# Performance work log

Hardware: AMD Instinct MI355X
Metric: run time of the kernel (lower is better)

Reference implementation:

```python
import jax, jax.numpy as jnp
import numpy as np

DIM = 768
HEADS = 12
HEAD_DIM = DIM // HEADS
HIDDEN = int(DIM * 2.0)
EPS = 1e-5


def layer_norm(x, g, b):
    mu = jnp.mean(x, axis=-1, keepdims=True)
    var = jnp.var(x, axis=-1, keepdims=True)
    return (x - mu) * jax.lax.rsqrt(var + EPS) * g + b


def setup_inputs() -> dict:
    key = jax.random.key(0)
    ks = jax.random.split(key, 10)
    B, N = 8, 1024
    s = 0.02
    return {
        "x": jax.random.normal(ks[0], (B, N, DIM), jnp.float32),
        "rpe_bias": jax.random.normal(ks[1], (HEADS, N, N), jnp.float32),
        # weights stored as (in, out); equals torch Linear weight transposed
        "qkv_w": jax.random.normal(ks[2], (DIM, 3 * DIM), jnp.float32) * s,
        "proj_w": jax.random.normal(ks[3], (DIM, DIM), jnp.float32) * s,
        "proj_b": jnp.zeros((DIM,), jnp.float32),
        "ln1_g": jnp.ones((DIM,), jnp.float32),
        "ln1_b": jnp.zeros((DIM,), jnp.float32),
        "ln2_g": jnp.ones((DIM,), jnp.float32),
        "ln2_b": jnp.zeros((DIM,), jnp.float32),
        "fc1_w": jax.random.normal(ks[4], (DIM, HIDDEN), jnp.float32) * s,
        "fc1_b": jnp.zeros((HIDDEN,), jnp.float32),
        "fc2_w": jax.random.normal(ks[5], (HIDDEN, DIM), jnp.float32) * s,
        "fc2_b": jnp.zeros((DIM,), jnp.float32),
    }


def reference(x, rpe_bias, qkv_w, proj_w, proj_b, ln1_g, ln1_b, ln2_g, ln2_b,
              fc1_w, fc1_b, fc2_w, fc2_b):
    B, N, C = x.shape
    scale = HEAD_DIM ** -0.5

    # ---- attention branch (pre-norm) ----
    h = layer_norm(x, ln1_g, ln1_b)
    qkv = h @ qkv_w                                   # [B,N,3C]
    qkv = qkv.reshape(B, N, 3, HEADS, HEAD_DIM)
    q = jnp.transpose(qkv[:, :, 0], (0, 2, 1, 3))     # [B,H,N,D]
    k = jnp.transpose(qkv[:, :, 1], (0, 2, 1, 3))
    v = jnp.transpose(qkv[:, :, 2], (0, 2, 1, 3))
    attn = jnp.einsum('bhnd,bhmd->bhnm', q, k) * scale + rpe_bias[None]
    attn = jax.nn.softmax(attn, axis=-1)
    o = jnp.einsum('bhnm,bhmd->bhnd', attn, v)        # [B,H,N,D]
    o = jnp.transpose(o, (0, 2, 1, 3)).reshape(B, N, C)
    x = x + (o @ proj_w + proj_b)

    # ---- MLP branch (pre-norm) ----
    h = layer_norm(x, ln2_g, ln2_b)
    h = jax.nn.gelu(h @ fc1_w + fc1_b, approximate=False)
    x = x + (h @ fc2_w + fc2_b)
    return x
```

## Files before the change

kernel.cpp:

```cpp
#include <hip/hip_runtime.h>

typedef __bf16 bf16;
typedef __bf16 bf16x8 __attribute__((ext_vector_type(8)));
typedef float f32x4 __attribute__((ext_vector_type(4)));

#define DIM 768
#define HEADS 12
#define HD 64
#define HIDDEN 1536
#define BB 8
#define NN 1024
#define ROWS (BB*NN)

__device__ __forceinline__ void gload_lds16(const void* g, void* l) {
  __builtin_amdgcn_global_load_lds(
      (const __attribute__((address_space(1))) void*)g,
      (__attribute__((address_space(3))) void*)l, 16, 0, 0);
}

__global__ __launch_bounds__(256) void rpe_cvt_kernel(
    const float* __restrict__ in, bf16* __restrict__ out)
{
  const size_t total = (size_t)HEADS * NN * NN;
  const size_t stride = (size_t)gridDim.x * 256 * 4;
  for (size_t i = ((size_t)blockIdx.x * 256 + threadIdx.x) * 4; i < total; i += stride) {
    const float4 v = *(const float4*)(in + i);
    ushort4 u;
    u.x = __builtin_bit_cast(unsigned short, (bf16)v.x);
    u.y = __builtin_bit_cast(unsigned short, (bf16)v.y);
    u.z = __builtin_bit_cast(unsigned short, (bf16)v.z);
    u.w = __builtin_bit_cast(unsigned short, (bf16)v.w);
    *(ushort4*)(out + i) = u;
  }
}

__global__ __launch_bounds__(256) void ln_kernel(
    const float* __restrict__ x, const float* __restrict__ gw,
    const float* __restrict__ bw, bf16* __restrict__ out)
{
  const int row = blockIdx.x;
  const int tid = threadIdx.x;
  const float* xr = x + (size_t)row * DIM;
  float v0 = xr[tid], v1 = xr[tid + 256], v2 = xr[tid + 512];
  float s1 = v0 + v1 + v2;
  float s2 = v0*v0 + v1*v1 + v2*v2;
#pragma unroll
  for (int off = 1; off < 64; off <<= 1) {
    s1 += __shfl_xor(s1, off);
    s2 += __shfl_xor(s2, off);
  }
  __shared__ float red[8];
  const int w = tid >> 6, lane = tid & 63;
  if (lane == 0) { red[w] = s1; red[4 + w] = s2; }
  __syncthreads();
  s1 = red[0] + red[1] + red[2] + red[3];
  s2 = red[4] + red[5] + red[6] + red[7];
  const float mu = s1 * (1.f / DIM);
  const float rstd = rsqrtf(s2 * (1.f / DIM) - mu * mu + 1e-5f);
  bf16* orow = out + (size_t)row * DIM;
  orow[tid]       = (bf16)((v0 - mu) * rstd * gw[tid]       + bw[tid]);
  orow[tid + 256] = (bf16)((v1 - mu) * rstd * gw[tid + 256] + bw[tid + 256]);
  orow[tid + 512] = (bf16)((v2 - mu) * rstd * gw[tid + 512] + bw[tid + 512]);
}

__global__ void wtrans_kernel(const float* __restrict__ in, bf16* __restrict__ out,
                              int K, int N)
{
  __shared__ float t[32][33];
  const int tx = threadIdx.x, ty = threadIdx.y;
  const int n0 = blockIdx.x * 32, k0 = blockIdx.y * 32;
#pragma unroll
  for (int i = 0; i < 32; i += 8)
    t[ty + i][tx] = in[(size_t)(k0 + ty + i) * N + n0 + tx];
  __syncthreads();
#pragma unroll
  for (int i = 0; i < 32; i += 8)
    out[(size_t)(n0 + ty + i) * K + k0 + tx] = (bf16)t[tx][ty + i];
}

template<int EPI>
__global__ __launch_bounds__(256, 2) void gemm128(
    const bf16* __restrict__ A, const bf16* __restrict__ Bt,
    int M, int N, int K,
    const float* __restrict__ bias, const float* __restrict__ resid,
    void* __restrict__ o0, void* __restrict__ o1, void* __restrict__ o2)
{
  __shared__ bf16 sA[128 * 64];
  __shared__ bf16 sB[128 * 64];
  const int tid = threadIdx.x;
  const int lane = tid & 63, w = tid >> 6;
  const int wrow = w >> 1, wcol = w & 1;
  const int m0 = blockIdx.y * 128, n0 = blockIdx.x * 128;
  const int l15 = lane & 15, l4 = lane >> 4;

  f32x4 acc[4][4] = {};

  const int crow = lane >> 3;
  const int cbyte = (lane & 7) * 16;
  const int ksteps = K >> 6;
  for (int kt = 0; kt < ksteps; ++kt) {
    const int k0 = kt << 6;
    __syncthreads();
#pragma unroll
    for (int c2 = 0; c2 < 4; ++c2) {
      const int c = (w << 2) + c2;
      const int r = (c << 3) + crow;
      gload_lds16((const char*)(A + (size_t)(m0 + r) * K + k0) + cbyte,
                  (char*)sA + c * 1024);
      gload_lds16((const char*)(Bt + (size_t)(n0 + r) * K + k0) + cbyte,
                  (char*)sB + c * 1024);
    }
    __syncthreads();
#pragma unroll
    for (int kk = 0; kk < 64; kk += 32) {
      bf16x8 af[4], bfv[4];
#pragma unroll
      for (int mf = 0; mf < 4; ++mf)
        af[mf] = *(const bf16x8*)(sA + (wrow * 64 + mf * 16 + l15) * 64 + kk + l4 * 8);
#pragma unroll
      for (int nf = 0; nf < 4; ++nf)
        bfv[nf] = *(const bf16x8*)(sB + (wcol * 64 + nf * 16 + l15) * 64 + kk + l4 * 8);
#pragma unroll
      for (int mf = 0; mf < 4; ++mf)
#pragma unroll
        for (int nf = 0; nf < 4; ++nf)
          acc[mf][nf] = __builtin_amdgcn_mfma_f32_16x16x32_bf16(af[mf], bfv[nf], acc[mf][nf], 0, 0, 0);
    }
  }

#pragma unroll
  for (int mf = 0; mf < 4; ++mf) {
    const int rbase = m0 + wrow * 64 + mf * 16 + l4 * 4;
#pragma unroll
    for (int nf = 0; nf < 4; ++nf) {
      const int colbase = n0 + wcol * 64 + nf * 16;
      const int col = colbase + l15;
      if constexpr (EPI == 0) {
        const int seg = colbase / 768;
        const int hh_ = (colbase - seg * 768) >> 6;
        const int dd = (colbase & 63) + l15;
        const int b_ = rbase >> 10;
        const int ns = rbase & 1023;
        const size_t gh = (size_t)(b_ * HEADS + hh_);
        bf16* Qb = (bf16*)o0; bf16* Kb = (bf16*)o1; bf16* Vtb = (bf16*)o2;
        if (seg == 0) {
#pragma unroll
          for (int rg = 0; rg < 4; ++rg)
            Qb[(gh * NN + ns + rg) * HD + dd] = (bf16)(acc[mf][nf][rg] * 0.125f);
        } else if (seg == 1) {
#pragma unroll
          for (int rg = 0; rg < 4; ++rg)
            Kb[(gh * NN + ns + rg) * HD + dd] = (bf16)acc[mf][nf][rg];
        } else {
          union { ushort4 u4; unsigned short us[4]; } pk;
#pragma unroll
          for (int rg = 0; rg < 4; ++rg)
            pk.us[rg] = __builtin_bit_cast(unsigned short, (bf16)acc[mf][nf][rg]);
          *(ushort4*)(Vtb + (gh * HD + dd) * NN + ns) = pk.u4;
        }
      } else if constexpr (EPI == 1 || EPI == 3) {
        float* outp = (float*)o0;
#pragma unroll
        for (int rg = 0; rg < 4; ++rg) {
          const size_t idx = (size_t)(rbase + rg) * N + col;
          outp[idx] = acc[mf][nf][rg] + bias[col] + resid[idx];
        }
      } else {
        bf16* outp = (bf16*)o0;
#pragma unroll
        for (int rg = 0; rg < 4; ++rg) {
          float v = acc[mf][nf][rg] + bias[col];
          float gl = 0.5f * v * (1.0f + erff(v * 0.70710678118654752f));
          outp[(size_t)(rbase + rg) * N + col] = (bf16)gl;
        }
      }
    }
  }
}

__global__ __launch_bounds__(256, 4) void attn_kernel(
    const bf16* __restrict__ Qb, const bf16* __restrict__ Kb,
    const bf16* __restrict__ Vtb, const bf16* __restrict__ rpeb,
    bf16* __restrict__ o_attn)
{
  __shared__ bf16 sK[2][64 * 64];
  __shared__ bf16 sV[2][64 * 64];
  __shared__ bf16 sP[4 * 16 * 64];
  const int tid = threadIdx.x;
  const int lane = tid & 63, w = tid >> 6;
  const int l15 = lane & 15, l4 = lane >> 4;
  const int bid = blockIdx.x;
  const int g = bid >> 4, qt = bid & 15;
  const int b_ = g / HEADS, h_ = g % HEADS;
  const int qbase = qt * 64 + w * 16;

  bf16x8 qf[2];
  {
    const bf16* qp = Qb + ((size_t)g * NN + qbase + l15) * HD + l4 * 8;
    qf[0] = *(const bf16x8*)qp;
    qf[1] = *(const bf16x8*)(qp + 32);
  }

  f32x4 oacc[4] = {};
  float m_r[4] = {-1e30f, -1e30f, -1e30f, -1e30f};
  float l_r[4] = {};
  const bf16* rpe_h = rpeb + (size_t)h_ * NN * NN;

  const int crow = lane >> 3;
  const int scol = ((lane & 7) * 16) ^ ((crow & 7) << 4);
  const int cc = w * 2;

#define STAGE(buf, kv0s) do {                                                      \
    _Pragma("unroll")                                                              \
    for (int c2 = 0; c2 < 2; ++c2) {                                               \
      const int c = cc + c2;                                                       \
      const int r = c * 8 + crow;                                                  \
      gload_lds16((const char*)(Kb + ((size_t)g * NN + (kv0s)) * HD) + r * 128 + scol, \
                  (char*)sK[buf] + c * 1024);                                      \
      gload_lds16((const char*)(Vtb + ((size_t)g * HD + r) * NN + (kv0s)) + scol,  \
                  (char*)sV[buf] + c * 1024);                                      \
    } } while (0)

  STAGE(0, 0);
  __syncthreads();
  int cur = 0;

  for (int kv0 = 0; kv0 < NN; kv0 += 64) {
    if (kv0 + 64 < NN) STAGE(cur ^ 1, kv0 + 64);

    float rv[4][4];
#pragma unroll
    for (int nf = 0; nf < 4; ++nf)
#pragma unroll
      for (int rg = 0; rg < 4; ++rg)
        rv[nf][rg] = (float)rpe_h[(size_t)(qbase + l4 * 4 + rg) * NN + kv0 + nf * 16 + l15];

    f32x4 s[4] = {};
#pragma unroll
    for (int kh = 0; kh < 2; ++kh) {
#pragma unroll
      for (int nf = 0; nf < 4; ++nf) {
        const int n_ = nf * 16 + l15;
        const bf16x8 kf = *(const bf16x8*)((const char*)sK[cur] + n_ * 128 +
                            (((kh * 32 + l4 * 8) * 2) ^ ((n_ & 7) << 4)));
        s[nf] = __builtin_amdgcn_mfma_f32_16x16x32_bf16(qf[kh], kf, s[nf], 0, 0, 0);
      }
    }
    float rm[4] = {-1e30f, -1e30f, -1e30f, -1e30f};
#pragma unroll
    for (int nf = 0; nf < 4; ++nf)
#pragma unroll
      for (int rg = 0; rg < 4; ++rg) {
        float v = s[nf][rg] + rv[nf][rg];
        s[nf][rg] = v;
        rm[rg] = fmaxf(rm[rg], v);
      }
#pragma unroll
    for (int off = 1; off <= 8; off <<= 1)
#pragma unroll
      for (int rg = 0; rg < 4; ++rg)
        rm[rg] = fmaxf(rm[rg], __shfl_xor(rm[rg], off));
    float al[4];
#pragma unroll
    for (int rg = 0; rg < 4; ++rg) {
      const float mn = fmaxf(m_r[rg], rm[rg]);
      al[rg] = __expf(m_r[rg] - mn);
      m_r[rg] = mn;
    }
    float rs[4] = {};
#pragma unroll
    for (int nf = 0; nf < 4; ++nf)
#pragma unroll
      for (int rg = 0; rg < 4; ++rg) {
        const float p = __expf(s[nf][rg] - m_r[rg]);
        rs[rg] += p;
        const int r = l4 * 4 + rg;
        const int cb = (nf * 16 + l15) * 2;
        *(bf16*)((char*)sP + w * 2048 + r * 128 + (cb ^ ((r & 7) << 4))) = (bf16)p;
      }
#pragma unroll
    for (int off = 1; off <= 8; off <<= 1)
#pragma unroll
      for (int rg = 0; rg < 4; ++rg)
        rs[rg] += __shfl_xor(rs[rg], off);
#pragma unroll
    for (int rg = 0; rg < 4; ++rg)
      l_r[rg] = l_r[rg] * al[rg] + rs[rg];
#pragma unroll
    for (int df = 0; df < 4; ++df)
#pragma unroll
      for (int rg = 0; rg < 4; ++rg)
        oacc[df][rg] *= al[rg];

#pragma unroll
    for (int kh = 0; kh < 2; ++kh) {
      const bf16x8 pf = *(const bf16x8*)((const char*)sP + w * 2048 + l15 * 128 +
                          (((kh * 32 + l4 * 8) * 2) ^ ((l15 & 7) << 4)));
#pragma unroll
      for (int df = 0; df < 4; ++df) {
        const int d_ = df * 16 + l15;
        const bf16x8 vf = *(const bf16x8*)((const char*)sV[cur] + d_ * 128 +
                            (((kh * 32 + l4 * 8) * 2) ^ ((d_ & 7) << 4)));
        oacc[df] = __builtin_amdgcn_mfma_f32_16x16x32_bf16(pf, vf, oacc[df], 0, 0, 0);
      }
    }
    __syncthreads();
    cur ^= 1;
  }
#undef STAGE

#pragma unroll
  for (int rg = 0; rg < 4; ++rg) {
    const float inv = 1.0f / l_r[rg];
    const int qr = qbase + l4 * 4 + rg;
    bf16* orow = o_attn + ((size_t)(b_ * NN) + qr) * DIM + h_ * HD;
#pragma unroll
    for (int df = 0; df < 4; ++df)
      orow[df * 16 + l15] = (bf16)(oacc[df][rg] * inv);
  }
}

extern "C" void kernel_launch(void* const* d_in, const int* in_sizes, int n_in,
                              void* d_out, int out_size, void* d_ws, size_t ws_size,
                              hipStream_t stream)
{
  const float* x      = (const float*)d_in[0];
  const float* rpe    = (const float*)d_in[1];
  const float* qkv_w  = (const float*)d_in[2];
  const float* proj_w = (const float*)d_in[3];
  const float* proj_b = (const float*)d_in[4];
  const float* ln1_g  = (const float*)d_in[5];
  const float* ln1_b  = (const float*)d_in[6];
  const float* ln2_g  = (const float*)d_in[7];
  const float* ln2_b  = (const float*)d_in[8];
  const float* fc1_w  = (const float*)d_in[9];
  const float* fc1_b  = (const float*)d_in[10];
  const float* fc2_w  = (const float*)d_in[11];
  const float* fc2_b  = (const float*)d_in[12];
  float* out = (float*)d_out;

  char* ws = (char*)d_ws;
  size_t off = 0;
  bf16* qkv_wT  = (bf16*)(ws + off); off += (size_t)2304 * 768 * 2;
  bf16* proj_wT = (bf16*)(ws + off); off += (size_t)768 * 768 * 2;
  bf16* fc1_wT  = (bf16*)(ws + off); off += (size_t)1536 * 768 * 2;
  bf16* fc2_wT  = (bf16*)(ws + off); off += (size_t)768 * 1536 * 2;
  bf16* hbuf    = (bf16*)(ws + off); off += (size_t)ROWS * DIM * 2;
  bf16* Qb      = (bf16*)(ws + off); off += (size_t)96 * NN * HD * 2;
  bf16* Kb      = (bf16*)(ws + off); off += (size_t)96 * NN * HD * 2;
  bf16* Vtb     = (bf16*)(ws + off); off += (size_t)96 * HD * NN * 2;
  float* x1     = (float*)(ws + off); off += (size_t)ROWS * DIM * 4;
  bf16* o_attn = hbuf;
  bf16* h2 = Qb;
  bf16* hh = Kb;
  bf16* rpeb = (bf16*)x1;

  dim3 tb(32, 8);
  wtrans_kernel<<<dim3(2304 / 32, 768 / 32), tb, 0, stream>>>(qkv_w, qkv_wT, 768, 2304);
  wtrans_kernel<<<dim3(768 / 32, 768 / 32),  tb, 0, stream>>>(proj_w, proj_wT, 768, 768);
  wtrans_kernel<<<dim3(1536 / 32, 768 / 32), tb, 0, stream>>>(fc1_w, fc1_wT, 768, 1536);
  wtrans_kernel<<<dim3(768 / 32, 1536 / 32), tb, 0, stream>>>(fc2_w, fc2_wT, 1536, 768);
  rpe_cvt_kernel<<<3072, 256, 0, stream>>>(rpe, rpeb);

  ln_kernel<<<ROWS, 256, 0, stream>>>(x, ln1_g, ln1_b, hbuf);
  gemm128<0><<<dim3(2304 / 128, ROWS / 128), 256, 0, stream>>>(
      hbuf, qkv_wT, ROWS, 2304, 768, nullptr, nullptr, (void*)Qb, (void*)Kb, (void*)Vtb);
  attn_kernel<<<96 * 16, 256, 0, stream>>>(Qb, Kb, Vtb, rpeb, o_attn);
  gemm128<1><<<dim3(768 / 128, ROWS / 128), 256, 0, stream>>>(
      o_attn, proj_wT, ROWS, 768, 768, proj_b, x, (void*)x1, nullptr, nullptr);
  ln_kernel<<<ROWS, 256, 0, stream>>>(x1, ln2_g, ln2_b, h2);
  gemm128<2><<<dim3(1536 / 128, ROWS / 128), 256, 0, stream>>>(
      h2, fc1_wT, ROWS, 1536, 768, fc1_b, nullptr, (void*)hh, nullptr, nullptr);
  gemm128<3><<<dim3(768 / 128, ROWS / 128), 256, 0, stream>>>(
      hh, fc2_wT, ROWS, 768, 1536, fc2_b, x1, (void*)out, nullptr, nullptr);
}
```

Baseline: 399.3 us.

## Prefetch RPE bias one tile ahead and unroll attention loop by two

The attention loop now loads the next tile's rpe bias values into registers during the current tile, using an A/B register ping-pong with a 2x unrolled loop so buffer indices are compile-time constants. This hides the global-load latency of the bias reads that previously stalled before the softmax. It also adds s_setprio around the MFMA sections and raises the GEMM launch bounds to 3 blocks per CU, which puts more pressure on registers and may cause spills.

```diff
diff --git a/kernel.cpp b/kernel.cpp
--- a/kernel.cpp
+++ b/kernel.cpp
@@ -79,7 +79,7 @@
 }
 
 template<int EPI>
-__global__ __launch_bounds__(256, 2) void gemm128(
+__global__ __launch_bounds__(256, 3) void gemm128(
     const bf16* __restrict__ A, const bf16* __restrict__ Bt,
     int M, int N, int K,
     const float* __restrict__ bias, const float* __restrict__ resid,
@@ -204,11 +204,13 @@
   f32x4 oacc[4] = {};
   float m_r[4] = {-1e30f, -1e30f, -1e30f, -1e30f};
   float l_r[4] = {};
-  const bf16* rpe_h = rpeb + (size_t)h_ * NN * NN;
+  const unsigned short* rpe_h = (const unsigned short*)(rpeb + (size_t)h_ * NN * NN);
 
   const int crow = lane >> 3;
   const int scol = ((lane & 7) * 16) ^ ((crow & 7) << 4);
   const int cc = w * 2;
+
+  unsigned short rvA[16], rvB[16];
 
 #define STAGE(buf, kv0s) do {                                                      \
     _Pragma("unroll")                                                              \
@@ -221,92 +223,100 @@
                   (char*)sV[buf] + c * 1024);                                      \
     } } while (0)
 
+#define RPE_LOAD(dst, kvs) do {                                                    \
+    _Pragma("unroll")                                                              \
+    for (int nf = 0; nf < 4; ++nf)                                                 \
+    _Pragma("unroll")                                                              \
+      for (int rg = 0; rg < 4; ++rg)                                               \
+        dst[nf * 4 + rg] = rpe_h[(size_t)(qbase + l4 * 4 + rg) * NN + (kvs) + nf * 16 + l15]; \
+    } while (0)
+
+#define TILE_BODY(buf, rvu, rvn, kv0c, kvn) do {                                   \
+    if ((kvn) < NN) { STAGE((buf) ^ 1, kvn); RPE_LOAD(rvn, kvn); }                 \
+    f32x4 s[4] = {};                                                               \
+    __builtin_amdgcn_s_setprio(1);                                                 \
+    _Pragma("unroll")                                                              \
+    for (int kh = 0; kh < 2; ++kh)                                                 \
+    _Pragma("unroll")                                                              \
+      for (int nf = 0; nf < 4; ++nf) {                                             \
+        const int n_ = nf * 16 + l15;                                              \
+        const bf16x8 kf = *(const bf16x8*)((const char*)sK[buf] + n_ * 128 +       \
+                            (((kh * 32 + l4 * 8) * 2) ^ ((n_ & 7) << 4)));         \
+        s[nf] = __builtin_amdgcn_mfma_f32_16x16x32_bf16(qf[kh], kf, s[nf], 0, 0, 0); \
+      }                                                                            \
+    __builtin_amdgcn_s_setprio(0);                                                 \
+    float rm[4] = {-1e30f, -1e30f, -1e30f, -1e30f};                                \
+    _Pragma("unroll")                                                              \
+    for (int nf = 0; nf < 4; ++nf)                                                 \
+    _Pragma("unroll")                                                              \
+      for (int rg = 0; rg < 4; ++rg) {                                             \
+        float v = s[nf][rg] + (float)__builtin_bit_cast(bf16, rvu[nf * 4 + rg]);   \
+        s[nf][rg] = v;                                                             \
+        rm[rg] = fmaxf(rm[rg], v);                                                 \
+      }                                                                            \
+    _Pragma("unroll")                                                              \
+    for (int off = 1; off <= 8; off <<= 1)                                         \
+    _Pragma("unroll")                                                              \
+      for (int rg = 0; rg < 4; ++rg)                                               \
+        rm[rg] = fmaxf(rm[rg], __shfl_xor(rm[rg], off));                           \
+    float al[4];                                                                   \
+    _Pragma("unroll")                                                              \
+    for (int rg = 0; rg < 4; ++rg) {                                               \
+      const float mn = fmaxf(m_r[rg], rm[rg]);                                     \
+      al[rg] = __expf(m_r[rg] - mn);                                               \
+      m_r[rg] = mn;                                                                \
+    }                                                                              \
+    float rs[4] = {};                                                              \
+    _Pragma("unroll")                                                              \
+    for (int nf = 0; nf < 4; ++nf)                                                 \
+    _Pragma("unroll")                                                              \
+      for (int rg = 0; rg < 4; ++rg) {                                             \
+        const float p = __expf(s[nf][rg] - m_r[rg]);                               \
+        rs[rg] += p;                                                               \
+        const int r = l4 * 4 + rg;                                                 \
+        const int cb = (nf * 16 + l15) * 2;                                        \
+        *(bf16*)((char*)sP + w * 2048 + r * 128 + (cb ^ ((r & 7) << 4))) = (bf16)p; \
+      }                                                                            \
+    _Pragma("unroll")                                                              \
+    for (int off = 1; off <= 8; off <<= 1)                                         \
+    _Pragma("unroll")                                                              \
+      for (int rg = 0; rg < 4; ++rg)                                               \
+        rs[rg] += __shfl_xor(rs[rg], off);                                         \
+    _Pragma("unroll")                                                              \
+    for (int rg = 0; rg < 4; ++rg)                                                 \
+      l_r[rg] = l_r[rg] * al[rg] + rs[rg];                                         \
+    _Pragma("unroll")                                                              \
+    for (int df = 0; df < 4; ++df)                                                 \
+    _Pragma("unroll")                                                              \
+      for (int rg = 0; rg < 4; ++rg)                                               \
+        oacc[df][rg] *= al[rg];                                                    \
+    __builtin_amdgcn_s_setprio(1);                                                 \
+    _Pragma("unroll")                                                              \
+    for (int kh = 0; kh < 2; ++kh) {                                               \
+      const bf16x8 pf = *(const bf16x8*)((const char*)sP + w * 2048 + l15 * 128 +  \
+                          (((kh * 32 + l4 * 8) * 2) ^ ((l15 & 7) << 4)));          \
+      _Pragma("unroll")                                                            \
+      for (int df = 0; df < 4; ++df) {                                             \
+        const int d_ = df * 16 + l15;                                              \
+        const bf16x8 vf = *(const bf16x8*)((const char*)sV[buf] + d_ * 128 +       \
+                            (((kh * 32 + l4 * 8) * 2) ^ ((d_ & 7) << 4)));         \
+        oacc[df] = __builtin_amdgcn_mfma_f32_16x16x32_bf16(pf, vf, oacc[df], 0, 0, 0); \
+      }                                                                            \
+    }                                                                              \
+    __builtin_amdgcn_s_setprio(0);                                                 \
+    __syncthreads();                                                               \
+  } while (0)
+
   STAGE(0, 0);
+  RPE_LOAD(rvA, 0);
   __syncthreads();
-  int cur = 0;
-
-  for (int kv0 = 0; kv0 < NN; kv0 += 64) {
-    if (kv0 + 64 < NN) STAGE(cur ^ 1, kv0 + 64);
-
-    float rv[4][4];
-#pragma unroll
-    for (int nf = 0; nf < 4; ++nf)
-#pragma unroll
-      for (int rg = 0; rg < 4; ++rg)
-        rv[nf][rg] = (float)rpe_h[(size_t)(qbase + l4 * 4 + rg) * NN + kv0 + nf * 16 + l15];
-
-    f32x4 s[4] = {};
-#pragma unroll
-    for (int kh = 0; kh < 2; ++kh) {
-#pragma unroll
-      for (int nf = 0; nf < 4; ++nf) {
-        const int n_ = nf * 16 + l15;
-        const bf16x8 kf = *(const bf16x8*)((const char*)sK[cur] + n_ * 128 +
-                            (((kh * 32 + l4 * 8) * 2) ^ ((n_ & 7) << 4)));
-        s[nf] = __builtin_amdgcn_mfma_f32_16x16x32_bf16(qf[kh], kf, s[nf], 0, 0, 0);
-      }
-    }
-    float rm[4] = {-1e30f, -1e30f, -1e30f, -1e30f};
-#pragma unroll
-    for (int nf = 0; nf < 4; ++nf)
-#pragma unroll
-      for (int rg = 0; rg < 4; ++rg) {
-        float v = s[nf][rg] + rv[nf][rg];
-        s[nf][rg] = v;
-        rm[rg] = fmaxf(rm[rg], v);
-      }
-#pragma unroll
-    for (int off = 1; off <= 8; off <<= 1)
-#pragma unroll
-      for (int rg = 0; rg < 4; ++rg)
-        rm[rg] = fmaxf(rm[rg], __shfl_xor(rm[rg], off));
-    float al[4];
-#pragma unroll
-    for (int rg = 0; rg < 4; ++rg) {
-      const float mn = fmaxf(m_r[rg], rm[rg]);
-      al[rg] = __expf(m_r[rg] - mn);
-      m_r[rg] = mn;
-    }
-    float rs[4] = {};
-#pragma unroll
-    for (int nf = 0; nf < 4; ++nf)
-#pragma unroll
-      for (int rg = 0; rg < 4; ++rg) {
-        const float p = __expf(s[nf][rg] - m_r[rg]);
-        rs[rg] += p;
-        const int r = l4 * 4 + rg;
-        const int cb = (nf * 16 + l15) * 2;
-        *(bf16*)((char*)sP + w * 2048 + r * 128 + (cb ^ ((r & 7) << 4))) = (bf16)p;
-      }
-#pragma unroll
-    for (int off = 1; off <= 8; off <<= 1)
-#pragma unroll
-      for (int rg = 0; rg < 4; ++rg)
-        rs[rg] += __shfl_xor(rs[rg], off);
-#pragma unroll
-    for (int rg = 0; rg < 4; ++rg)
-      l_r[rg] = l_r[rg] * al[rg] + rs[rg];
-#pragma unroll
-    for (int df = 0; df < 4; ++df)
-#pragma unroll
-      for (int rg = 0; rg < 4; ++rg)
-        oacc[df][rg] *= al[rg];
-
-#pragma unroll
-    for (int kh = 0; kh < 2; ++kh) {
-      const bf16x8 pf = *(const bf16x8*)((const char*)sP + w * 2048 + l15 * 128 +
-                          (((kh * 32 + l4 * 8) * 2) ^ ((l15 & 7) << 4)));
-#pragma unroll
-      for (int df = 0; df < 4; ++df) {
-        const int d_ = df * 16 + l15;
-        const bf16x8 vf = *(const bf16x8*)((const char*)sV[cur] + d_ * 128 +
-                            (((kh * 32 + l4 * 8) * 2) ^ ((d_ & 7) << 4)));
-        oacc[df] = __builtin_amdgcn_mfma_f32_16x16x32_bf16(pf, vf, oacc[df], 0, 0, 0);
-      }
-    }
-    __syncthreads();
-    cur ^= 1;
-  }
+
+  for (int kv0 = 0; kv0 < NN; kv0 += 128) {
+    TILE_BODY(0, rvA, rvB, kv0, kv0 + 64);
+    TILE_BODY(1, rvB, rvA, kv0 + 64, kv0 + 128);
+  }
+#undef TILE_BODY
+#undef RPE_LOAD
 #undef STAGE
 
 #pragma unroll
```

After: 552.4 us. 1.38x slower.
